# Kernel tuning notes

Hardware: AMD Instinct MI355X
Metric: run time of the kernel (lower is better)

The kernel has to match this reference:

```python
import jax, jax.numpy as jnp
import numpy as np


def setup_inputs() -> dict:
    key = jax.random.key(0)
    ks = jax.random.split(key, 16)
    N, F_in, C, E = 50000, 128, 64, 800000
    H = 2 * C      # hidden width of first GCN layer = 128
    P = 128        # num_proj_hidden
    K = 3          # cluster_num (hardcoded in GRACE)

    def lin(kw, fan_in, fan_out):
        # torch Linear default init: U(-1/sqrt(fan_in), 1/sqrt(fan_in))
        bound = 1.0 / np.sqrt(fan_in)
        return jax.random.uniform(kw, (fan_in, fan_out), jnp.float32, -bound, bound)

    inp = {
        "x1": jax.random.normal(ks[0], (N, F_in), jnp.float32),
        "edge_index1": jax.random.randint(ks[1], (2, E), 0, N, jnp.int64 if jax.config.jax_enable_x64 else jnp.int32),
        "x2": jax.random.normal(ks[2], (N, F_in), jnp.float32),
        "edge_index2": jax.random.randint(ks[3], (2, E), 0, N, jnp.int64 if jax.config.jax_enable_x64 else jnp.int32),
        # encoder GCN layers
        "W1": lin(ks[4], F_in, H), "b1": jnp.zeros((H,), jnp.float32),
        "W2": lin(ks[5], H, C),    "b2": jnp.zeros((C,), jnp.float32),
        # instance projector: Linear(C,C) -> ReLU -> Linear(C,P)
        "Wp1": lin(ks[6], C, C), "bp1": jnp.zeros((C,), jnp.float32),
        "Wp2": lin(ks[7], C, P), "bp2": jnp.zeros((P,), jnp.float32),
        # cluster projector: Linear(C,C) -> ReLU -> Linear(C,K) -> Softmax
        "Wc1": lin(ks[8], C, C), "bc1": jnp.zeros((C,), jnp.float32),
        "Wc2": lin(ks[9], C, K), "bc2": jnp.zeros((K,), jnp.float32),
    }
    return inp


def _gcn_encoder(x, edge_index, W1, b1, W2, b2):
    N = x.shape[0]
    loop = jnp.arange(N, dtype=edge_index.dtype)
    row = jnp.concatenate([edge_index[0], loop])  # message sources (x_j)
    col = jnp.concatenate([edge_index[1], loop])  # aggregation targets
    deg = jax.ops.segment_sum(jnp.ones_like(col, jnp.float32), col, num_segments=N)
    dinv = jax.lax.rsqrt(deg)  # deg >= 1 due to self loops
    norm = dinv[row] * dinv[col]  # [E+N]

    def layer(h, W, b):
        h = h @ W  # transform first (PyG GCNConv), [N, F_out]
        msg = h[row] * norm[:, None]  # gather + scale, [E+N, F_out]
        return jax.ops.segment_sum(msg, col, num_segments=N) + b

    h = jax.nn.relu(layer(x, W1, b1))
    h = jax.nn.relu(layer(h, W2, b2))
    return h


def _l2norm(z, eps=1e-12):
    # matches F.normalize(z, dim=1): x / max(||x||, eps)
    n = jnp.sqrt(jnp.sum(z * z, axis=1, keepdims=True))
    return z / jnp.maximum(n, eps)


def reference(x1, edge_index1, x2, edge_index2,
              W1, b1, W2, b2, Wp1, bp1, Wp2, bp2, Wc1, bc1, Wc2, bc2):
    z1 = _gcn_encoder(x1, edge_index1, W1, b1, W2, b2)
    z2 = _gcn_encoder(x2, edge_index2, W1, b1, W2, b2)

    inst = lambda z: _l2norm(jax.nn.relu(z @ Wp1 + bp1) @ Wp2 + bp2)
    clus = lambda z: jax.nn.softmax(jax.nn.relu(z @ Wc1 + bc1) @ Wc2 + bc2, axis=1)

    z_i = inst(z1)
    z_j = inst(z2)
    c_i = clus(z1)
    c_j = clus(z2)
    return (z_i, z_j, c_i, c_j)
```

## Files before the change

kernel.cpp:

```cpp
#include <hip/hip_runtime.h>
#include <cstdint>
#include <cstddef>

using u16 = unsigned short;
using u32 = unsigned int;

typedef __bf16 bf16x8 __attribute__((ext_vector_type(8)));
typedef float  f32x4  __attribute__((ext_vector_type(4)));

__device__ __forceinline__ float bf2f(u16 b) { union { u32 i; float f; } v; v.i = ((u32)b) << 16; return v.f; }
__device__ __forceinline__ u16 f2bf(float f) { __bf16 b = (__bf16)f; return __builtin_bit_cast(u16, b); }
__device__ __forceinline__ float bflo(u32 u) { union { u32 i; float f; } v; v.i = u << 16; return v.f; }
__device__ __forceinline__ float bfhi(u32 u) { union { u32 i; float f; } v; v.i = u & 0xffff0000u; return v.f; }
__device__ __forceinline__ u32 pack2(float a, float b) { return (u32)f2bf(a) | ((u32)f2bf(b) << 16); }

__device__ __forceinline__ float loadx(const void* p, size_t i, int flag_bf16) {
    return flag_bf16 ? bf2f(((const u16*)p)[i]) : ((const float*)p)[i];
}
__device__ __forceinline__ void storex(void* p, size_t i, float v, int flag_bf16) {
    if (flag_bf16) ((u16*)p)[i] = f2bf(v);
    else           ((float*)p)[i] = v;
}

__device__ __forceinline__ bf16x8 load_afrag_ext(const void* A, size_t off, int flag) {
    if (flag) return *reinterpret_cast<const bf16x8*>((const u16*)A + off);
    const float* f = (const float*)A + off;
    float4 a = *reinterpret_cast<const float4*>(f);
    float4 b = *reinterpret_cast<const float4*>(f + 4);
    bf16x8 r;
    r[0] = (__bf16)a.x; r[1] = (__bf16)a.y; r[2] = (__bf16)a.z; r[3] = (__bf16)a.w;
    r[4] = (__bf16)b.x; r[5] = (__bf16)b.y; r[6] = (__bf16)b.z; r[7] = (__bf16)b.w;
    return r;
}

__global__ void k_detect(const u32* __restrict__ x, int* __restrict__ flag) {
    int lane = threadIdx.x;
    u32 u = x[lane];
    int e = (u >> 7) & 0xFF;
    int hit = (e >= 100 && e <= 145) ? 1 : 0;
    unsigned long long b = __ballot(hit);
    if (lane == 0) flag[0] = (__popcll(b) >= 32) ? 1 : 0;
}

struct ConvJob { const void* src; float* dst; int n; };
struct ConvJobs { ConvJob j[12]; };

__global__ void k_wconv(ConvJobs jobs, const int* __restrict__ flagp) {
    const int f = *flagp;
    const int stride = gridDim.x * blockDim.x;
    for (int s = 0; s < 12; ++s) {
        const ConvJob jb = jobs.j[s];
        for (int i = blockIdx.x * blockDim.x + threadIdx.x; i < jb.n; i += stride)
            jb.dst[i] = loadx(jb.src, i, f);
    }
}

struct TJob { const float* W; u16* WT; int K, NC; };
struct TJobs { TJob j[5]; };

__global__ void k_wtrans(TJobs jobs) {
    const int stride = gridDim.x * blockDim.x;
    for (int s = 0; s < 5; ++s) {
        const TJob jb = jobs.j[s];
        const int tot = jb.K * jb.NC;
        for (int i = blockIdx.x * blockDim.x + threadIdx.x; i < tot; i += stride) {
            int k = i / jb.NC, n = i - k * jb.NC;
            jb.WT[n * jb.K + k] = f2bf(jb.W[i]);
        }
    }
}

static const int CAPSH = 9;
static const int OVCAP = 65536;

__global__ __launch_bounds__(256) void k_bin(const int* __restrict__ ei0, const int* __restrict__ ei1,
                                             int* __restrict__ cnt, u32* __restrict__ bins,
                                             int2* __restrict__ ov, int* __restrict__ ocnt,
                                             int N, int E, int NB) {
    const int g = blockIdx.y;
    const int xcd = blockIdx.x & 7;
    const int* ei = g ? ei1 : ei0;
    const int per = (E + gridDim.x - 1) / gridDim.x;
    const int e0 = blockIdx.x * per;
    const int e1 = (e0 + per < E) ? e0 + per : E;
    int* c = cnt + (size_t)(g * 8 + xcd) * NB;
    u32* bs = bins + ((size_t)(g * 8 + xcd) * NB << CAPSH);
    for (int e = e0 + threadIdx.x; e < e1; e += 256) {
        int s = __builtin_nontemporal_load(ei + e);
        int d = __builtin_nontemporal_load(ei + E + e);
        int b = d >> 7;
        int pos = atomicAdd(&c[b], 1);
        if (pos < (1 << CAPSH)) {
            bs[((size_t)b << CAPSH) + pos] = (u32)s | ((u32)(d & 127) << 16);
        } else {
            int oi = atomicAdd(ocnt, 1);
            if (oi < OVCAP) ov[oi] = make_int2(s, d | (g << 24));
        }
    }
}

__global__ __launch_bounds__(256) void k_bscan(const int* __restrict__ cnt, const int2* __restrict__ ov,
                                               const int* __restrict__ ocnt, int* __restrict__ bbase,
                                               int* __restrict__ rowptr, int N, int E, int NB) {
    __shared__ int tot[2][512];
    const int tid = threadIdx.x;
    for (int g = 0; g < 2; ++g)
        for (int i = tid; i < 512; i += 256) {
            int s = 0;
            if (i < NB)
                for (int x = 0; x < 8; ++x) {
                    int cv = cnt[(size_t)(g * 8 + x) * NB + i];
                    s += (cv < (1 << CAPSH)) ? cv : (1 << CAPSH);
                }
            tot[g][i] = s;
        }
    __syncthreads();
    int no = *ocnt; if (no > OVCAP) no = OVCAP;
    for (int i = tid; i < no; i += 256) {
        int y = ov[i].y;
        atomicAdd(&tot[y >> 24][(y & 0xFFFFFF) >> 7], 1);
    }
    __syncthreads();
    int o00 = tot[0][tid], o01 = tot[0][tid + 256];
    int o10 = tot[1][tid], o11 = tot[1][tid + 256];
    for (int off = 1; off < 512; off <<= 1) {
        int a0 = tot[0][tid]       + ((tid >= off)       ? tot[0][tid - off]       : 0);
        int a1 = tot[0][tid + 256] + ((tid + 256 >= off) ? tot[0][tid + 256 - off] : 0);
        int b0 = tot[1][tid]       + ((tid >= off)       ? tot[1][tid - off]       : 0);
        int b1 = tot[1][tid + 256] + ((tid + 256 >= off) ? tot[1][tid + 256 - off] : 0);
        __syncthreads();
        tot[0][tid] = a0; tot[0][tid + 256] = a1;
        tot[1][tid] = b0; tot[1][tid + 256] = b1;
        __syncthreads();
    }
    if (tid < NB)       { bbase[tid]            = tot[0][tid] - o00;       bbase[NB + tid]       = tot[1][tid] - o10; }
    if (tid + 256 < NB) { bbase[tid + 256]      = tot[0][tid + 256] - o01; bbase[NB + tid + 256] = tot[1][tid + 256] - o11; }
    if (tid == 0) {
        rowptr[N] = E;
        rowptr[(size_t)(N + 1) + N] = E;
    }
}

__global__ __launch_bounds__(256) void k_scatter(const int* __restrict__ cnt, const u32* __restrict__ bins,
                                                 const int2* __restrict__ ov, const int* __restrict__ ocnt,
                                                 const int* __restrict__ bbase, int* __restrict__ rowptr,
                                                 float* __restrict__ dinv, int* __restrict__ csr,
                                                 int N, int E, int NB) {
    const int g = blockIdx.y, b = blockIdx.x, tid = threadIdx.x;
    const int lo = b << 7;
    int R = N - lo; if (R > 128) R = 128;
    __shared__ int hist[128], scn[128], cur[128];
    if (tid < 128) hist[tid] = 0;
    __syncthreads();
    int segn[8];
    const u32* segp[8];
#pragma unroll
    for (int x = 0; x < 8; ++x) {
        size_t cell = (size_t)(g * 8 + x) * NB + b;
        int cv = cnt[cell];
        segn[x] = (cv < (1 << CAPSH)) ? cv : (1 << CAPSH);
        segp[x] = bins + (cell << CAPSH);
    }
#pragma unroll
    for (int x = 0; x < 8; ++x)
        for (int i = tid; i < segn[x]; i += 256)
            atomicAdd(&hist[segp[x][i] >> 16], 1);
    int no = *ocnt; if (no > OVCAP) no = OVCAP;
    for (int i = tid; i < no; i += 256) {
        int y = ov[i].y;
        if ((y >> 24) != g) continue;
        int d = y & 0xFFFFFF;
        if (d >= lo && d < lo + 128) atomicAdd(&hist[d - lo], 1);
    }
    __syncthreads();
    int orig = (tid < 128) ? hist[tid] : 0;
    if (tid < 128) scn[tid] = orig;
    __syncthreads();
    for (int off = 1; off < 128; off <<= 1) {
        int v = 0;
        if (tid < 128) v = scn[tid] + ((tid >= off) ? scn[tid - off] : 0);
        __syncthreads();
        if (tid < 128) scn[tid] = v;
        __syncthreads();
    }
    const int base = bbase[g * NB + b];
    if (tid < R) {
        int ex = base + scn[tid] - orig;
        rowptr[(size_t)g * (N + 1) + lo + tid] = ex;
        cur[tid] = ex;
        dinv[(size_t)g * N + lo + tid] = rsqrtf((float)(orig + 1));
    }
    __syncthreads();
    int* out = csr + (size_t)g * E;
#pragma unroll
    for (int x = 0; x < 8; ++x)
        for (int i = tid; i < segn[x]; i += 256) {
            u32 v = segp[x][i];
            int pos = atomicAdd(&cur[v >> 16], 1);
            out[pos] = (int)(v & 0xFFFFu);
        }
    for (int i = tid; i < no; i += 256) {
        int y = ov[i].y;
        if ((y >> 24) != g) continue;
        int d = y & 0xFFFFFF;
        if (d >= lo && d < lo + 128) {
            int pos = atomicAdd(&cur[d - lo], 1);
            out[pos] = ov[i].x;
        }
    }
}

template <int K, int NC, bool AEXT, bool BIAS, bool RELU, bool NORM, bool OEXT>
__global__ __launch_bounds__(256) void k_mgemm(const void* __restrict__ A0, const void* __restrict__ A1,
                                               size_t astride, const u16* __restrict__ WT,
                                               const float* __restrict__ bias, void* __restrict__ outv,
                                               size_t out_off, size_t ostride, int M,
                                               const int* __restrict__ flagp) {
    constexpr int NT = NC / 16;
    constexpr int KI = K / 32;
    const int flag = *flagp;
    const int g = blockIdx.y;
    const void* Av = g ? A1 : A0;
    const int lane = threadIdx.x & 63;
    const int wave = threadIdx.x >> 6;
    const int q = lane >> 4;
    const int c = lane & 15;
    const int m0 = blockIdx.x * 64 + wave * 16;
    int arow = m0 + c;
    if (arow > M - 1) arow = M - 1;
    const size_t abase = (size_t)g * astride + (size_t)arow * K;

    bf16x8 afr[KI];
#pragma unroll
    for (int ki = 0; ki < KI; ++ki) {
        size_t off = abase + (size_t)ki * 32 + q * 8;
        if (AEXT) afr[ki] = load_afrag_ext(Av, off, flag);
        else      afr[ki] = *reinterpret_cast<const bf16x8*>((const u16*)Av + off);
    }

    f32x4 acc[NT];
#pragma unroll
    for (int t = 0; t < NT; ++t) acc[t] = (f32x4){0.f, 0.f, 0.f, 0.f};

#pragma unroll
    for (int ki = 0; ki < KI; ++ki) {
#pragma unroll
        for (int t = 0; t < NT; ++t) {
            const u16* bptr = WT + (size_t)(t * 16 + c) * K + ki * 32 + q * 8;
            bf16x8 bfr = *reinterpret_cast<const bf16x8*>(bptr);
            acc[t] = __builtin_amdgcn_mfma_f32_16x16x32_bf16(afr[ki], bfr, acc[t], 0, 0, 0);
        }
    }

#pragma unroll
    for (int t = 0; t < NT; ++t) {
        float bv = BIAS ? bias[t * 16 + c] : 0.f;
#pragma unroll
        for (int r = 0; r < 4; ++r) {
            float v = acc[t][r] + bv;
            if (RELU) v = fmaxf(v, 0.f);
            acc[t][r] = v;
        }
    }

    if constexpr (NORM) {
        float ss[4] = {0.f, 0.f, 0.f, 0.f};
#pragma unroll
        for (int t = 0; t < NT; ++t)
#pragma unroll
            for (int r = 0; r < 4; ++r) ss[r] += acc[t][r] * acc[t][r];
#pragma unroll
        for (int r = 0; r < 4; ++r) {
#pragma unroll
            for (int m = 1; m < 16; m <<= 1) ss[r] += __shfl_xor(ss[r], m, 64);
            float s = 1.f / fmaxf(sqrtf(ss[r]), 1e-12f);
#pragma unroll
            for (int t = 0; t < NT; ++t) acc[t][r] *= s;
        }
    }

    const size_t obase = out_off + (size_t)g * ostride;
#pragma unroll
    for (int r = 0; r < 4; ++r) {
        const int grow = m0 + q * 4 + r;
        if (grow < M) {
#pragma unroll
            for (int t = 0; t < NT; ++t) {
                size_t oi = obase + (size_t)grow * NC + t * 16 + c;
                if (OEXT) storex(outv, oi, acc[t][r], flag);
                else      ((u16*)outv)[oi] = f2bf(acc[t][r]);
            }
        }
    }
}

__global__ __launch_bounds__(256) void k_agg128(const u32* __restrict__ H, const int* __restrict__ rowptr,
                                                const int* __restrict__ csr, const float* __restrict__ dinv,
                                                const float* __restrict__ bias, u32* __restrict__ out,
                                                int N, int E) {
    const int g = blockIdx.y;
    const int node = blockIdx.x * 4 + (threadIdx.x >> 6);
    if (node >= N) return;
    const int lane = threadIdx.x & 63;
    const u32* h = H + (size_t)g * N * 64;
    const int* rp = rowptr + (size_t)g * (N + 1);
    const int* cs = csr + (size_t)g * E;
    const float* dv = dinv + (size_t)g * N;
    const float dn = dv[node];
    int e = rp[node];
    const int end = rp[node + 1];
    u32 su = h[(size_t)node * 64 + lane];
    float w = dn * dn;
    float a0 = bflo(su) * w, a1 = bfhi(su) * w;
    while (e + 8 <= end) {
        int sx[8];
#pragma unroll
        for (int j = 0; j < 8; ++j) sx[j] = cs[e + j];
        u32 hv[8]; float ws[8];
#pragma unroll
        for (int j = 0; j < 8; ++j) { hv[j] = h[(size_t)sx[j] * 64 + lane]; ws[j] = dv[sx[j]]; }
#pragma unroll
        for (int j = 0; j < 8; ++j) {
            float wj = ws[j] * dn;
            a0 += bflo(hv[j]) * wj;
            a1 += bfhi(hv[j]) * wj;
        }
        e += 8;
    }
    while (e + 2 <= end) {
        int s0 = cs[e], s1 = cs[e + 1];
        u32 h0 = h[(size_t)s0 * 64 + lane];
        u32 h1 = h[(size_t)s1 * 64 + lane];
        float w0 = dv[s0] * dn, w1 = dv[s1] * dn;
        a0 += bflo(h0) * w0; a1 += bfhi(h0) * w0;
        a0 += bflo(h1) * w1; a1 += bfhi(h1) * w1;
        e += 2;
    }
    if (e < end) {
        int s0 = cs[e];
        float w0 = dv[s0] * dn;
        u32 h0 = h[(size_t)s0 * 64 + lane];
        a0 += bflo(h0) * w0; a1 += bfhi(h0) * w0;
    }
    a0 = fmaxf(a0 + bias[2 * lane], 0.f);
    a1 = fmaxf(a1 + bias[2 * lane + 1], 0.f);
    out[((size_t)g * N + node) * 64 + lane] = pack2(a0, a1);
}

__global__ __launch_bounds__(256) void k_agg64(const u16* __restrict__ H, const int* __restrict__ rowptr,
                                               const int* __restrict__ csr, const float* __restrict__ dinv,
                                               const float* __restrict__ bias, u16* __restrict__ out,
                                               int N, int E) {
    const int g = blockIdx.y;
    const int node = blockIdx.x * 4 + (threadIdx.x >> 6);
    if (node >= N) return;
    const int lane = threadIdx.x & 63;
    const u16* h = H + (size_t)g * N * 64;
    const int* rp = rowptr + (size_t)g * (N + 1);
    const int* cs = csr + (size_t)g * E;
    const float* dv = dinv + (size_t)g * N;
    const float dn = dv[node];
    int e = rp[node];
    const int end = rp[node + 1];
    float a0 = bf2f(h[(size_t)node * 64 + lane]) * dn * dn;
    while (e + 8 <= end) {
        int sx[8];
#pragma unroll
        for (int j = 0; j < 8; ++j) sx[j] = cs[e + j];
        u16 hv[8]; float ws[8];
#pragma unroll
        for (int j = 0; j < 8; ++j) { hv[j] = h[(size_t)sx[j] * 64 + lane]; ws[j] = dv[sx[j]]; }
#pragma unroll
        for (int j = 0; j < 8; ++j) a0 += bf2f(hv[j]) * (ws[j] * dn);
        e += 8;
    }
    while (e + 2 <= end) {
        int s0 = cs[e], s1 = cs[e + 1];
        float h0 = bf2f(h[(size_t)s0 * 64 + lane]);
        float h1 = bf2f(h[(size_t)s1 * 64 + lane]);
        a0 += h0 * (dv[s0] * dn) + h1 * (dv[s1] * dn);
        e += 2;
    }
    if (e < end) {
        int s0 = cs[e];
        a0 += bf2f(h[(size_t)s0 * 64 + lane]) * (dv[s0] * dn);
    }
    a0 = fmaxf(a0 + bias[lane], 0.f);
    out[((size_t)g * N + node) * 64 + lane] = f2bf(a0);
}

__global__ __launch_bounds__(256) void k_clus(const u16* __restrict__ v, const float* __restrict__ Wc2,
                                              const float* __restrict__ bc2, void* __restrict__ outv,
                                              size_t out_off, size_t ostride, int N,
                                              const int* __restrict__ flagp) {
    const int g = blockIdx.y;
    const int node = blockIdx.x * 4 + (threadIdx.x >> 6);
    if (node >= N) return;
    const int flag = *flagp;
    const int lane = threadIdx.x & 63;
    float ul = bf2f(v[((size_t)g * N + node) * 64 + lane]);
    float a0 = ul * Wc2[lane * 3 + 0];
    float a1 = ul * Wc2[lane * 3 + 1];
    float a2 = ul * Wc2[lane * 3 + 2];
#pragma unroll
    for (int m = 1; m < 64; m <<= 1) {
        a0 += __shfl_xor(a0, m, 64);
        a1 += __shfl_xor(a1, m, 64);
        a2 += __shfl_xor(a2, m, 64);
    }
    a0 += bc2[0]; a1 += bc2[1]; a2 += bc2[2];
    float mx = fmaxf(a0, fmaxf(a1, a2));
    float e0 = expf(a0 - mx), e1 = expf(a1 - mx), e2 = expf(a2 - mx);
    float inv = 1.f / (e0 + e1 + e2);
    if (lane < 3) {
        float r = (lane == 0) ? e0 : ((lane == 1) ? e1 : e2);
        storex(outv, out_off + (size_t)g * ostride + (size_t)node * 3 + lane, r * inv, flag);
    }
}

extern "C" void kernel_launch(void* const* d_in, const int* in_sizes, int n_in,
                              void* d_out, int out_size, void* d_ws, size_t ws_size,
                              hipStream_t stream) {
    const int N = in_sizes[0] / 128;
    const int E = in_sizes[1] / 2;
    const int* ei0 = (const int*)d_in[1];
    const int* ei1 = (const int*)d_in[3];
    const int NB = (N + 127) >> 7;

    size_t off = 0;
    auto alloc = [&](size_t bytes) -> void* {
        void* p = (char*)d_ws + off;
        off += (bytes + 255) & ~(size_t)255;
        return p;
    };
    int* flag = (int*)alloc(256);
    const int wcnt[12] = {128 * 128, 128, 128 * 64, 64, 64 * 64, 64, 64 * 128, 128, 64 * 64, 64, 64 * 3, 3};
    float* wf[12];
    for (int i = 0; i < 12; ++i) wf[i] = (float*)alloc((size_t)wcnt[i] * 4);
    float* b1f = wf[1]; float* b2f = wf[3]; float* bp1f = wf[5]; float* bp2f = wf[7];
    float* bc1f = wf[9]; float* Wc2f = wf[10]; float* bc2f = wf[11];
    u16* W1T  = (u16*)alloc(128 * 128 * 2);
    u16* W2T  = (u16*)alloc(64 * 128 * 2);
    u16* Wp1T = (u16*)alloc(64 * 64 * 2);
    u16* Wp2T = (u16*)alloc(128 * 64 * 2);
    u16* Wc1T = (u16*)alloc(64 * 64 * 2);

    const int ncell = 2 * 8 * NB;
    int* cnt    = (int*)alloc((size_t)(ncell + 1) * 4);
    int* ocnt   = cnt + ncell;
    int2* ov    = (int2*)alloc((size_t)OVCAP * 8);
    u32* bins   = (u32*)alloc(((size_t)ncell << CAPSH) * 4);
    int* bbase  = (int*)alloc((size_t)2 * NB * 4);
    int* rowptr = (int*)alloc((size_t)2 * (N + 1) * 4);
    float* dinv = (float*)alloc((size_t)2 * N * 4);
    int* csr    = (int*)alloc((size_t)2 * E * 4);
    u16* A1 = (u16*)alloc((size_t)2 * N * 128 * 2);
    u16* H2 = A1;
    u16* Qb = (u16*)alloc((size_t)2 * N * 128 * 2);
    u16* U  = Qb;
    u16* Z  = (u16*)alloc((size_t)2 * N * 64 * 2);
    (void)ws_size; (void)n_in; (void)out_size;

    k_detect<<<1, 64, 0, stream>>>((const u32*)d_in[0], flag);
    ConvJobs jobs;
    for (int i = 0; i < 12; ++i) jobs.j[i] = ConvJob{d_in[4 + i], wf[i], wcnt[i]};
    k_wconv<<<64, 256, 0, stream>>>(jobs, flag);
    TJobs tj;
    tj.j[0] = TJob{wf[0], W1T, 128, 128};
    tj.j[1] = TJob{wf[2], W2T, 128, 64};
    tj.j[2] = TJob{wf[4], Wp1T, 64, 64};
    tj.j[3] = TJob{wf[6], Wp2T, 64, 128};
    tj.j[4] = TJob{wf[8], Wc1T, 64, 64};
    k_wtrans<<<40, 256, 0, stream>>>(tj);

    hipMemsetAsync(cnt, 0, (size_t)(ncell + 1) * 4, stream);
    k_bin<<<dim3(512, 2), 256, 0, stream>>>(ei0, ei1, cnt, bins, ov, ocnt, N, E, NB);
    k_bscan<<<1, 256, 0, stream>>>(cnt, ov, ocnt, bbase, rowptr, N, E, NB);
    k_scatter<<<dim3(NB, 2), 256, 0, stream>>>(cnt, bins, ov, ocnt, bbase, rowptr, dinv, csr, N, E, NB);

    const dim3 gM((N + 63) / 64, 2);
    const dim3 gA((N + 3) / 4, 2);

    k_mgemm<128, 128, true, false, false, false, false><<<gM, 256, 0, stream>>>(
        d_in[0], d_in[2], 0, W1T, nullptr, A1, 0, (size_t)N * 128, N, flag);
    k_agg128<<<gA, 256, 0, stream>>>((const u32*)A1, rowptr, csr, dinv, b1f, (u32*)Qb, N, E);
    k_mgemm<128, 64, false, false, false, false, false><<<gM, 256, 0, stream>>>(
        Qb, Qb, (size_t)N * 128, W2T, nullptr, H2, 0, (size_t)N * 64, N, flag);
    k_agg64<<<gA, 256, 0, stream>>>(H2, rowptr, csr, dinv, b2f, Z, N, E);

    k_mgemm<64, 64, false, true, true, false, false><<<gM, 256, 0, stream>>>(
        Z, Z, (size_t)N * 64, Wp1T, bp1f, U, 0, (size_t)N * 64, N, flag);
    k_mgemm<64, 128, false, true, false, true, true><<<gM, 256, 0, stream>>>(
        U, U, (size_t)N * 64, Wp2T, bp2f, d_out, 0, (size_t)N * 128, N, flag);
    k_mgemm<64, 64, false, true, true, false, false><<<gM, 256, 0, stream>>>(
        Z, Z, (size_t)N * 64, Wc1T, bc1f, U, 0, (size_t)N * 64, N, flag);
    k_clus<<<gA, 256, 0, stream>>>(U, Wc2f, bc2f, d_out,
                                   (size_t)2 * N * 128, (size_t)N * 3, N, flag);
}
```

Measured before the change: 490.0 us.

## Replace per-XCD global atomic binning with block-local histogram and bulk reservation

```diff
diff --git a/kernel.cpp b/kernel.cpp
--- a/kernel.cpp
+++ b/kernel.cpp
@@ -70,28 +70,42 @@
     }
 }
 
-static const int CAPSH = 9;
+static const int CAPSH = 12;
 static const int OVCAP = 65536;
 
 __global__ __launch_bounds__(256) void k_bin(const int* __restrict__ ei0, const int* __restrict__ ei1,
-                                             int* __restrict__ cnt, u32* __restrict__ bins,
+                                             int* __restrict__ cur, u32* __restrict__ stage,
                                              int2* __restrict__ ov, int* __restrict__ ocnt,
-                                             int N, int E, int NB) {
+                                             int E, int NB, int nblk) {
     const int g = blockIdx.y;
-    const int xcd = blockIdx.x & 7;
     const int* ei = g ? ei1 : ei0;
-    const int per = (E + gridDim.x - 1) / gridDim.x;
-    const int e0 = blockIdx.x * per;
-    const int e1 = (e0 + per < E) ? e0 + per : E;
-    int* c = cnt + (size_t)(g * 8 + xcd) * NB;
-    u32* bs = bins + ((size_t)(g * 8 + xcd) * NB << CAPSH);
-    for (int e = e0 + threadIdx.x; e < e1; e += 256) {
+    const int chunk = (E + nblk - 1) / nblk;
+    const int e0 = blockIdx.x * chunk;
+    const int e1 = (e0 + chunk < E) ? e0 + chunk : E;
+    const int tid = threadIdx.x;
+    __shared__ int h[512];
+    __shared__ int lb[512];
+    for (int i = tid; i < NB; i += 256) h[i] = 0;
+    __syncthreads();
+    for (int e = e0 + tid; e < e1; e += 256) {
+        int d = __builtin_nontemporal_load(ei + E + e);
+        atomicAdd(&h[d >> 7], 1);
+    }
+    __syncthreads();
+    for (int b = tid; b < NB; b += 256) {
+        int c = h[b];
+        lb[b] = c ? atomicAdd(&cur[g * NB + b], c) : 0;
+    }
+    __syncthreads();
+    for (int i = tid; i < NB; i += 256) h[i] = 0;
+    __syncthreads();
+    for (int e = e0 + tid; e < e1; e += 256) {
         int s = __builtin_nontemporal_load(ei + e);
-        int d = __builtin_nontemporal_load(ei + E + e);
+        int d = ei[E + e];
         int b = d >> 7;
-        int pos = atomicAdd(&c[b], 1);
-        if (pos < (1 << CAPSH)) {
-            bs[((size_t)b << CAPSH) + pos] = (u32)s | ((u32)(d & 127) << 16);
+        int p = lb[b] + atomicAdd(&h[b], 1);
+        if (p < (1 << CAPSH)) {
+            stage[((size_t)(g * NB + b) << CAPSH) + p] = (u32)s | ((u32)(d & 127) << 16);
         } else {
             int oi = atomicAdd(ocnt, 1);
             if (oi < OVCAP) ov[oi] = make_int2(s, d | (g << 24));
@@ -99,7 +113,7 @@
     }
 }
 
-__global__ __launch_bounds__(256) void k_bscan(const int* __restrict__ cnt, const int2* __restrict__ ov,
+__global__ __launch_bounds__(256) void k_bscan(const int* __restrict__ cur, const int2* __restrict__ ov,
                                                const int* __restrict__ ocnt, int* __restrict__ bbase,
                                                int* __restrict__ rowptr, int N, int E, int NB) {
     __shared__ int tot[2][512];
@@ -107,11 +121,10 @@
     for (int g = 0; g < 2; ++g)
         for (int i = tid; i < 512; i += 256) {
             int s = 0;
-            if (i < NB)
-                for (int x = 0; x < 8; ++x) {
-                    int cv = cnt[(size_t)(g * 8 + x) * NB + i];
-                    s += (cv < (1 << CAPSH)) ? cv : (1 << CAPSH);
-                }
+            if (i < NB) {
+                int cv = cur[g * NB + i];
+                s = (cv < (1 << CAPSH)) ? cv : (1 << CAPSH);
+            }
             tot[g][i] = s;
         }
     __syncthreads();
@@ -141,7 +154,7 @@
     }
 }
 
-__global__ __launch_bounds__(256) void k_scatter(const int* __restrict__ cnt, const u32* __restrict__ bins,
+__global__ __launch_bounds__(256) void k_scatter(const int* __restrict__ cur, const u32* __restrict__ stage,
                                                  const int2* __restrict__ ov, const int* __restrict__ ocnt,
                                                  const int* __restrict__ bbase, int* __restrict__ rowptr,
                                                  float* __restrict__ dinv, int* __restrict__ csr,
@@ -149,22 +162,13 @@
     const int g = blockIdx.y, b = blockIdx.x, tid = threadIdx.x;
     const int lo = b << 7;
     int R = N - lo; if (R > 128) R = 128;
-    __shared__ int hist[128], scn[128], cur[128];
+    __shared__ int hist[128], scn[128], curs[128];
     if (tid < 128) hist[tid] = 0;
     __syncthreads();
-    int segn[8];
-    const u32* segp[8];
-#pragma unroll
-    for (int x = 0; x < 8; ++x) {
-        size_t cell = (size_t)(g * 8 + x) * NB + b;
-        int cv = cnt[cell];
-        segn[x] = (cv < (1 << CAPSH)) ? cv : (1 << CAPSH);
-        segp[x] = bins + (cell << CAPSH);
-    }
-#pragma unroll
-    for (int x = 0; x < 8; ++x)
-        for (int i = tid; i < segn[x]; i += 256)
-            atomicAdd(&hist[segp[x][i] >> 16], 1);
+    int cv = cur[g * NB + b];
+    const int n = (cv < (1 << CAPSH)) ? cv : (1 << CAPSH);
+    const u32* sp = stage + ((size_t)(g * NB + b) << CAPSH);
+    for (int i = tid; i < n; i += 256) atomicAdd(&hist[sp[i] >> 16], 1);
     int no = *ocnt; if (no > OVCAP) no = OVCAP;
     for (int i = tid; i < no; i += 256) {
         int y = ov[i].y;
@@ -187,24 +191,22 @@
     if (tid < R) {
         int ex = base + scn[tid] - orig;
         rowptr[(size_t)g * (N + 1) + lo + tid] = ex;
-        cur[tid] = ex;
+        curs[tid] = ex;
         dinv[(size_t)g * N + lo + tid] = rsqrtf((float)(orig + 1));
     }
     __syncthreads();
     int* out = csr + (size_t)g * E;
-#pragma unroll
-    for (int x = 0; x < 8; ++x)
-        for (int i = tid; i < segn[x]; i += 256) {
-            u32 v = segp[x][i];
-            int pos = atomicAdd(&cur[v >> 16], 1);
-            out[pos] = (int)(v & 0xFFFFu);
-        }
+    for (int i = tid; i < n; i += 256) {
+        u32 v = sp[i];
+        int pos = atomicAdd(&curs[v >> 16], 1);
+        out[pos] = (int)(v & 0xFFFFu);
+    }
     for (int i = tid; i < no; i += 256) {
         int y = ov[i].y;
         if ((y >> 24) != g) continue;
         int d = y & 0xFFFFFF;
         if (d >= lo && d < lo + 128) {
-            int pos = atomicAdd(&cur[d - lo], 1);
+            int pos = atomicAdd(&curs[d - lo], 1);
             out[pos] = ov[i].x;
         }
     }
@@ -445,11 +447,11 @@
     u16* Wp2T = (u16*)alloc(128 * 64 * 2);
     u16* Wc1T = (u16*)alloc(64 * 64 * 2);
 
-    const int ncell = 2 * 8 * NB;
-    int* cnt    = (int*)alloc((size_t)(ncell + 1) * 4);
-    int* ocnt   = cnt + ncell;
+    const int ncell = 2 * NB;
+    int* cur    = (int*)alloc((size_t)(ncell + 1) * 4);
+    int* ocnt   = cur + ncell;
     int2* ov    = (int2*)alloc((size_t)OVCAP * 8);
-    u32* bins   = (u32*)alloc(((size_t)ncell << CAPSH) * 4);
+    u32* stage  = (u32*)alloc(((size_t)ncell << CAPSH) * 4);
     int* bbase  = (int*)alloc((size_t)2 * NB * 4);
     int* rowptr = (int*)alloc((size_t)2 * (N + 1) * 4);
     float* dinv = (float*)alloc((size_t)2 * N * 4);
@@ -473,10 +475,11 @@
     tj.j[4] = TJob{wf[8], Wc1T, 64, 64};
     k_wtrans<<<40, 256, 0, stream>>>(tj);
 
-    hipMemsetAsync(cnt, 0, (size_t)(ncell + 1) * 4, stream);
-    k_bin<<<dim3(512, 2), 256, 0, stream>>>(ei0, ei1, cnt, bins, ov, ocnt, N, E, NB);
-    k_bscan<<<1, 256, 0, stream>>>(cnt, ov, ocnt, bbase, rowptr, N, E, NB);
-    k_scatter<<<dim3(NB, 2), 256, 0, stream>>>(cnt, bins, ov, ocnt, bbase, rowptr, dinv, csr, N, E, NB);
+    hipMemsetAsync(cur, 0, (size_t)(ncell + 1) * 4, stream);
+    const int NBLK = 128;
+    k_bin<<<dim3(NBLK, 2), 256, 0, stream>>>(ei0, ei1, cur, stage, ov, ocnt, E, NB, NBLK);
+    k_bscan<<<1, 256, 0, stream>>>(cur, ov, ocnt, bbase, rowptr, N, E, NB);
+    k_scatter<<<dim3(NB, 2), 256, 0, stream>>>(cur, stage, ov, ocnt, bbase, rowptr, dinv, csr, N, E, NB);
 
     const dim3 gM((N + 63) / 64, 2);
     const dim3 gA((N + 3) / 4, 2);
```

Measured after the change: 428.1 us. 1.14x faster.
